# Kernel tuning notes

Hardware: AMD Instinct MI355X
Metric: run time of the kernel (lower is better)

The kernel has to match this reference:

```python
import jax, jax.numpy as jnp
import numpy as np

B, DIM_IN, DIM_OUT, K, EMBED, N, S = 32, 32, 32, 2, 16, 2048, 12


def setup_inputs() -> dict:
    key = jax.random.key(0)
    ks = jax.random.split(key, 12)
    sc = 0.1
    return {
        "x": jax.random.normal(ks[0], (B, DIM_IN, N, S), dtype=jnp.float32),
        "node_embeddings": jax.random.normal(ks[1], (N, EMBED), dtype=jnp.float32),
        "node_embeddings2": jax.random.normal(ks[2], (N, EMBED), dtype=jnp.float32),
        "weights_pool": jax.random.normal(ks[3], (EMBED, K + 1, DIM_IN, DIM_OUT), dtype=jnp.float32) * sc,
        "weights_pool2": jax.random.normal(ks[4], (EMBED, K + 1, DIM_IN, DIM_OUT), dtype=jnp.float32) * sc,
        "bias_pool": jax.random.normal(ks[5], (EMBED, DIM_OUT), dtype=jnp.float32) * sc,
        "bias_pool2": jax.random.normal(ks[6], (EMBED, DIM_OUT), dtype=jnp.float32) * sc,
        "fc0_w": jax.random.normal(ks[7], (1, S), dtype=jnp.float32) * sc,
        "fc0_b": jnp.zeros((1,), dtype=jnp.float32),
        "fc1_w": jax.random.normal(ks[8], (EMBED, N), dtype=jnp.float32) * sc,
        "fc1_b": jnp.zeros((EMBED,), dtype=jnp.float32),
        "fc2_w": jax.random.normal(ks[9], (EMBED, DIM_IN), dtype=jnp.float32) * sc,
        "fc2_b": jnp.zeros((EMBED,), dtype=jnp.float32),
    }


def _mlp(x, fc0_w, fc0_b, fc1_w, fc1_b, fc2_w, fc2_b):
    # x: [B, i, n, s] -> use first batch element, as in the torch code
    h = x[0]                                        # [i, n, s]
    h = jnp.tanh((h @ fc0_w.T + fc0_b).squeeze(-1))  # [i, n]
    h = jnp.tanh(h @ fc1_w.T + fc1_b)                # [i, d]
    h = h.T                                          # [d, i]
    h = jnp.tanh(h @ fc2_w.T + fc2_b)                # [d, d]
    return h


def reference(x, node_embeddings, node_embeddings2, weights_pool, weights_pool2,
              bias_pool, bias_pool2, fc0_w, fc0_b, fc1_w, fc1_b, fc2_w, fc2_b):
    m = _mlp(x, fc0_w, fc0_b, fc1_w, fc1_b, fc2_w, fc2_b)          # [d, d]
    logits = jax.nn.relu((node_embeddings @ m) @ node_embeddings2.T)  # [n, n]
    support = jax.nn.softmax(logits, axis=1)                        # [n, n]

    # k-hop powers of the dynamic adjacency (k is a small static int)
    support_set = [jnp.eye(N, dtype=support.dtype)]
    for _ in range(K):
        support_set.append(support_set[-1] @ support)
    supports = jnp.stack(support_set, axis=0)                       # [K+1, n, n]

    # node-embedding-generated weights and bias
    weights = (jnp.einsum('nd,dkio->nkio', node_embeddings, weights_pool)
               + jnp.einsum('nd,dkio->nkio', node_embeddings2, weights_pool2))  # [n,K+1,i,o]
    bias = node_embeddings @ bias_pool + node_embeddings2 @ bias_pool2          # [n, o]

    x_g = jnp.einsum('knm,bims->bknis', supports, x)                # [b,K+1,n,i,s]
    x_gconv = jnp.einsum('bknis,nkio->bsno', x_g, weights) + bias   # [b,s,n,o]
    out = jnp.transpose(x_gconv, (0, 3, 2, 1))                      # [b,o,n,s]
    # dropout is identity in eval mode
    return out
```

## Files before the change

### kernel.cpp

```cpp
#include <hip/hip_runtime.h>


typedef float  f32x4  __attribute__((ext_vector_type(4)));
typedef __bf16 bf16x8 __attribute__((ext_vector_type(8)));
typedef unsigned short u16;

#define GLOAD16(gp, lp) __builtin_amdgcn_global_load_lds( \
    (const __attribute__((address_space(1))) void*)(gp),  \
    (__attribute__((address_space(3))) void*)(lp), 16, 0, 0)

__device__ __forceinline__ u16 f2bf(float f){
  union { float f; unsigned u; } v; v.f = f;
  unsigned u = v.u;
  u += 0x7fffu + ((u >> 16) & 1u);
  return (u16)(u >> 16);
}
__device__ __forceinline__ float bf2f(u16 h){
  union { unsigned u; float f; } v; v.u = ((unsigned)h) << 16;
  return v.f;
}
__device__ __forceinline__ float2 unp2(unsigned u){
  union { unsigned q; float f; } a, b;
  a.q = u << 16; b.q = u & 0xffff0000u;
  return make_float2(a.f, b.f);
}

__global__ void k_h1(const float* __restrict__ x, const float* __restrict__ fc0w,
                     const float* __restrict__ fc0b, float* __restrict__ h1){
  int g = blockIdx.x * 256 + threadIdx.x;
  const float* xp = x + (long)g * 12;
  float s = fc0b[0];
  #pragma unroll
  for (int j = 0; j < 12; j++) s += xp[j] * fc0w[j];
  h1[g] = tanhf(s);
}

__global__ __launch_bounds__(256) void k_h2a(const float* __restrict__ h1,
                                             const float* __restrict__ fc1w,
                                             float* __restrict__ h2raw){
  __shared__ float red[4];
  int id = blockIdx.x;
  int i = id >> 4, d = id & 15;
  int t = threadIdx.x;
  const float* hp = h1 + i * 2048;
  const float* wp = fc1w + d * 2048;
  float s = 0.f;
  for (int nn = t; nn < 2048; nn += 256) s += hp[nn] * wp[nn];
  for (int off = 32; off > 0; off >>= 1) s += __shfl_down(s, off, 64);
  if ((t & 63) == 0) red[t >> 6] = s;
  __syncthreads();
  if (t == 0) h2raw[id] = red[0] + red[1] + red[2] + red[3];
}

__global__ void k_h2b(const float* __restrict__ h2raw, const float* __restrict__ fc1b,
                      const float* __restrict__ fc2w, const float* __restrict__ fc2b,
                      float* __restrict__ mmat){
  __shared__ float h2[512];
  int t = threadIdx.x;
  {
    int d = t & 15;
    h2[t] = tanhf(h2raw[t] + fc1b[d]);
  }
  __syncthreads();
  if (t < 256){
    int dd = t >> 4, e = t & 15;
    float s2 = fc2b[e];
    #pragma unroll
    for (int ii = 0; ii < 32; ii++) s2 += h2[ii * 16 + dd] * fc2w[e * 32 + ii];
    mmat[dd * 16 + e] = tanhf(s2);
  }
}

__global__ __launch_bounds__(256) void k_support(const float* __restrict__ E1,
                                                 const float* __restrict__ E2,
                                                 const float* __restrict__ mmat,
                                                 u16* __restrict__ sup){
  __shared__ float ml[256];
  __shared__ float tv[16];
  __shared__ float red[8];
  int n = blockIdx.x, t = threadIdx.x;
  ml[t] = mmat[t];
  __syncthreads();
  if (t < 16){
    float s = 0.f;
    const float* er = E1 + n * 16;
    #pragma unroll
    for (int d = 0; d < 16; d++) s += er[d] * ml[d * 16 + t];
    tv[t] = s;
  }
  __syncthreads();
  float lmax = -1e30f;
  float lv[8];
  #pragma unroll
  for (int p = 0; p < 8; p++){
    int j = t + p * 256;
    const float* e2 = E2 + j * 16;
    float s = 0.f;
    #pragma unroll
    for (int d = 0; d < 16; d++) s += tv[d] * e2[d];
    s = fmaxf(s, 0.f);
    lv[p] = s;
    lmax = fmaxf(lmax, s);
  }
  for (int off = 32; off > 0; off >>= 1) lmax = fmaxf(lmax, __shfl_down(lmax, off, 64));
  if ((t & 63) == 0) red[t >> 6] = lmax;
  __syncthreads();
  if (t == 0) red[0] = fmaxf(fmaxf(red[0], red[1]), fmaxf(red[2], red[3]));
  __syncthreads();
  float mx = red[0];
  float lsum = 0.f;
  #pragma unroll
  for (int p = 0; p < 8; p++){ float e = __expf(lv[p] - mx); lv[p] = e; lsum += e; }
  for (int off = 32; off > 0; off >>= 1) lsum += __shfl_down(lsum, off, 64);
  if ((t & 63) == 0) red[4 + (t >> 6)] = lsum;
  __syncthreads();
  if (t == 0) red[4] = red[4] + red[5] + red[6] + red[7];
  __syncthreads();
  float inv = 1.f / red[4];
  #pragma unroll
  for (int p = 0; p < 8; p++) sup[(long)n * 2048 + t + p * 256] = f2bf(lv[p] * inv);
}

__global__ void k_xb(const float* __restrict__ x, u16* __restrict__ Xb){
  int idx = blockIdx.x * 256 + threadIdx.x;
  int m = idx / 12288;
  int c = idx - m * 12288;
  int bi = c / 12, s = c - bi * 12;
  Xb[idx] = f2bf(x[((long)bi * 2048 + m) * 12 + s]);
}

__global__ __launch_bounds__(256) void k_xbt(const u16* __restrict__ Xb,
                                             u16* __restrict__ Xbt){
  __shared__ u16 tile[64][65];
  int cT = blockIdx.x * 64;
  int mT = blockIdx.y * 64;
  int t = threadIdx.x;
  int r = t >> 6, cc = t & 63;
  #pragma unroll
  for (int p = 0; p < 16; p++){
    int rr = p * 4 + r;
    tile[rr][cc] = Xb[(long)(mT + rr) * 12288 + cT + cc];
  }
  __syncthreads();
  #pragma unroll
  for (int p = 0; p < 16; p++){
    int rr = p * 4 + r;
    Xbt[(long)(cT + rr) * 2048 + mT + cc] = tile[cc][rr];
  }
}

__global__ void k_wb(const float* __restrict__ E1, const float* __restrict__ E2,
                     const float* __restrict__ P1, const float* __restrict__ P2,
                     const float* __restrict__ BP1, const float* __restrict__ BP2,
                     float* __restrict__ W, float* __restrict__ biasN){
  long g = (long)blockIdx.x * 256 + threadIdx.x;
  const long NW = (long)2048 * 3072;
  if (g < NW){
    int n = (int)(g / 3072), r = (int)(g - (long)n * 3072);
    const float* e1 = E1 + n * 16; const float* e2 = E2 + n * 16;
    float s = 0.f;
    #pragma unroll
    for (int d = 0; d < 16; d++) s += e1[d] * P1[d * 3072 + r] + e2[d] * P2[d * 3072 + r];
    W[g] = s;
  } else {
    long e = g - NW;
    if (e < 2048 * 32){
      int n = (int)(e >> 5), o = (int)(e & 31);
      const float* e1 = E1 + n * 16; const float* e2 = E2 + n * 16;
      float s = 0.f;
      #pragma unroll
      for (int d = 0; d < 16; d++) s += e1[d] * BP1[d * 32 + o] + e2[d] * BP2[d * 32 + o];
      biasN[e] = s;
    }
  }
}

__global__ __launch_bounds__(256) void k_gemm(const u16* __restrict__ A,
                                              const u16* __restrict__ Bt,
                                              u16* __restrict__ Cd,
                                              u16* __restrict__ Ct,
                                              int writeT){
  __shared__ u16 As[128 * 32];
  __shared__ u16 Bs[128 * 32];
  int tid  = threadIdx.x;
  int wave = tid >> 6, lane = tid & 63;
  int l15 = lane & 15, q = lane >> 4;
  int wm = wave >> 1, wc = wave & 1;
  long mBase = (long)blockIdx.y * 128;
  long cBase = (long)blockIdx.x * 128;
  f32x4 acc[4][4];
  #pragma unroll
  for (int t = 0; t < 4; t++)
    #pragma unroll
    for (int u = 0; u < 4; u++) acc[t][u] = (f32x4){0.f, 0.f, 0.f, 0.f};

  const u16* gA = A  + (mBase + wave * 16 + (lane >> 2)) * 2048 + (lane & 3) * 8;
  const u16* gB = Bt + (cBase + wave * 16 + (lane >> 2)) * 2048 + (lane & 3) * 8;
  u16* lA0 = As + wave * 512;
  u16* lA1 = As + 2048 + wave * 512;
  u16* lB0 = Bs + wave * 512;
  u16* lB1 = Bs + 2048 + wave * 512;

  for (int k0 = 0; k0 < 2048; k0 += 32){
    __syncthreads();
    GLOAD16(gA + k0,              lA0);
    GLOAD16(gA + 64 * 2048 + k0,  lA1);
    GLOAD16(gB + k0,              lB0);
    GLOAD16(gB + 64 * 2048 + k0,  lB1);
    __syncthreads();
    bf16x8 a[4], b[4];
    #pragma unroll
    for (int t = 0; t < 4; t++)
      a[t] = *(const bf16x8*)&As[(wm * 64 + t * 16 + l15) * 32 + q * 8];
    #pragma unroll
    for (int u = 0; u < 4; u++)
      b[u] = *(const bf16x8*)&Bs[(wc * 64 + u * 16 + l15) * 32 + q * 8];
    #pragma unroll
    for (int t = 0; t < 4; t++)
      #pragma unroll
      for (int u = 0; u < 4; u++)
        acc[t][u] = __builtin_amdgcn_mfma_f32_16x16x32_bf16(a[t], b[u], acc[t][u], 0, 0, 0);
  }
  #pragma unroll
  for (int t = 0; t < 4; t++){
    int mloc = wm * 64 + t * 16 + q * 4;
    #pragma unroll
    for (int u = 0; u < 4; u++){
      int cloc = wc * 64 + u * 16 + l15;
      long cg = cBase + cloc;
      long mg = mBase + mloc;
      u16 h0 = f2bf(acc[t][u][0]);
      u16 h1v = f2bf(acc[t][u][1]);
      u16 h2v = f2bf(acc[t][u][2]);
      u16 h3v = f2bf(acc[t][u][3]);
      Cd[(mg + 0) * 12288 + cg] = h0;
      Cd[(mg + 1) * 12288 + cg] = h1v;
      Cd[(mg + 2) * 12288 + cg] = h2v;
      Cd[(mg + 3) * 12288 + cg] = h3v;
      if (writeT){
        ushort4 v = make_ushort4(h0, h1v, h2v, h3v);
        *(ushort4*)&Ct[cg * 2048 + mg] = v;
      }
    }
  }
}

__global__ __launch_bounds__(256, 4) void k_final(const u16* __restrict__ G0,
                                                  const u16* __restrict__ G1,
                                                  const u16* __restrict__ G2,
                                                  const float* __restrict__ W,
                                                  const float* __restrict__ biasN,
                                                  float* __restrict__ out){
  __shared__ __align__(16) u16 gs[32 * 400];
  __shared__ __align__(16) float ws4[1024];
  __shared__ float bbuf[32];
  int bid = blockIdx.x;
  int n = (bid & 7) * 256 + (bid >> 3);
  int t = threadIdx.x;
  int b = t >> 3, oc = t & 7;
  f32x4 acc[4][3];
  #pragma unroll
  for (int jo = 0; jo < 4; jo++)
    #pragma unroll
    for (int v = 0; v < 3; v++) acc[jo][v] = (f32x4){0.f, 0.f, 0.f, 0.f};

  const u16* srcs[3] = {G0, G1, G2};
  for (int k = 0; k < 3; k++){
    __syncthreads();
    const uint4* src = (const uint4*)(srcs[k] + (long)n * 12288);
    #pragma unroll
    for (int p = 0; p < 6; p++){
      int c = t + p * 256;
      int br = c / 48, wi = c - br * 48;
      *(uint4*)&gs[br * 400 + wi * 8] = src[c];
    }
    const float4* wsrc = (const float4*)(W + (long)n * 3072 + k * 1024);
    *(float4*)&ws4[t * 4] = wsrc[t];
    if (k == 0 && t < 8) *(float4*)&bbuf[t * 4] = ((const float4*)(biasN + (long)n * 32))[t];
    __syncthreads();

    const u16* gp = gs + b * 400;
    #pragma unroll 4
    for (int ii = 0; ii < 16; ii++){
      uint4 A  = *(const uint4*)&gp[ii * 24];
      uint4 Bc = *(const uint4*)&gp[ii * 24 + 8];
      uint4 Cc = *(const uint4*)&gp[ii * 24 + 16];
      float2 p0 = unp2(A.x),  p1 = unp2(A.y),  p2 = unp2(A.z),  p3 = unp2(A.w);
      float2 p4 = unp2(Bc.x), p5 = unp2(Bc.y), p6 = unp2(Bc.z), p7 = unp2(Bc.w);
      float2 p8 = unp2(Cc.x), p9 = unp2(Cc.y), pa = unp2(Cc.z), pb = unp2(Cc.w);
      f32x4 G0v0 = (f32x4){p0.x, p0.y, p1.x, p1.y};
      f32x4 G0v1 = (f32x4){p2.x, p2.y, p3.x, p3.y};
      f32x4 G0v2 = (f32x4){p4.x, p4.y, p5.x, p5.y};
      f32x4 G1v0 = (f32x4){p6.x, p6.y, p7.x, p7.y};
      f32x4 G1v1 = (f32x4){p8.x, p8.y, p9.x, p9.y};
      f32x4 G1v2 = (f32x4){pa.x, pa.y, pb.x, pb.y};
      #pragma unroll
      for (int jo = 0; jo < 4; jo++){
        float w0 = ws4[(ii * 2)     * 32 + oc + jo * 8];
        float w1 = ws4[(ii * 2 + 1) * 32 + oc + jo * 8];
        acc[jo][0] += G0v0 * w0;
        acc[jo][1] += G0v1 * w0;
        acc[jo][2] += G0v2 * w0;
        acc[jo][0] += G1v0 * w1;
        acc[jo][1] += G1v1 * w1;
        acc[jo][2] += G1v2 * w1;
      }
    }
  }
  #pragma unroll
  for (int jo = 0; jo < 4; jo++){
    int o = oc + jo * 8;
    float bv = bbuf[o];
    f32x4 bs = {bv, bv, bv, bv};
    long base = ((long)(b * 32 + o) * 2048 + n) * 12;
    *(f32x4*)(out + base)     = acc[jo][0] + bs;
    *(f32x4*)(out + base + 4) = acc[jo][1] + bs;
    *(f32x4*)(out + base + 8) = acc[jo][2] + bs;
  }
}

extern "C" void kernel_launch(void* const* d_in, const int* in_sizes, int n_in,
                              void* d_out, int out_size, void* d_ws, size_t ws_size,
                              hipStream_t stream){
  const float* x    = (const float*)d_in[0];
  const float* E1   = (const float*)d_in[1];
  const float* E2   = (const float*)d_in[2];
  const float* P1   = (const float*)d_in[3];
  const float* P2   = (const float*)d_in[4];
  const float* BP1  = (const float*)d_in[5];
  const float* BP2  = (const float*)d_in[6];
  const float* fc0w = (const float*)d_in[7];
  const float* fc0b = (const float*)d_in[8];
  const float* fc1w = (const float*)d_in[9];
  const float* fc1b = (const float*)d_in[10];
  const float* fc2w = (const float*)d_in[11];
  const float* fc2b = (const float*)d_in[12];
  float* out = (float*)d_out;

  char* ws = (char*)d_ws;
  size_t off = 0;
  auto carve = [&](size_t bytes) -> char* {
    char* p = ws + off;
    off += (bytes + 255) & ~(size_t)255;
    return p;
  };
  float* h1            = (float*)carve((size_t)65536 * 4);
  float* h2raw         = (float*)carve((size_t)512 * 4);
  float* mmat          = (float*)carve((size_t)256 * 4);
  u16* sup             = (u16*)carve((size_t)2048 * 2048 * 2);
  u16* Xbt             = (u16*)carve((size_t)12288 * 2048 * 2);
  u16* Xb              = (u16*)carve((size_t)2048 * 12288 * 2);
  u16* G1t             = (u16*)carve((size_t)12288 * 2048 * 2);
  u16* G1              = (u16*)carve((size_t)2048 * 12288 * 2);
  float* W             = (float*)carve((size_t)2048 * 3072 * 4);
  float* biasN         = (float*)carve((size_t)2048 * 32 * 4);
  u16* G2              = Xbt;
  (void)ws_size; (void)in_sizes; (void)n_in; (void)out_size;

  k_h1     <<<256, 256, 0, stream>>>(x, fc0w, fc0b, h1);
  k_h2a    <<<512, 256, 0, stream>>>(h1, fc1w, h2raw);
  k_h2b    <<<1, 512, 0, stream>>>(h2raw, fc1b, fc2w, fc2b, mmat);
  k_support<<<2048, 256, 0, stream>>>(E1, E2, mmat, sup);
  k_xb     <<<98304, 256, 0, stream>>>(x, Xb);
  k_xbt    <<<dim3(192, 32), 256, 0, stream>>>(Xb, Xbt);
  k_wb     <<<24832, 256, 0, stream>>>(E1, E2, P1, P2, BP1, BP2, W, biasN);
  k_gemm   <<<dim3(96, 16), 256, 0, stream>>>(sup, Xbt, G1, G1t, 1);
  k_gemm   <<<dim3(96, 16), 256, 0, stream>>>(sup, G1t, G2, G1t, 0);
  k_final  <<<2048, 256, 0, stream>>>(Xb, G1, G2, W, biasN, out);
}
```

Baseline: 683.3 us.

## Deepen GEMM K-step, remap blocks across XCDs, stage epilogue through LDS

The bf16 MFMA GEMM now loads a K-slab of 64 per iteration instead of 32, which halves the number of barrier pairs. Block indices are remapped so that neighbouring column tiles are spread across the 8 XCDs while blocks sharing A rows stay grouped, aimed at better L2 reuse. The output tile is staged in a padded LDS buffer so that both the direct and transposed results go out as 16-byte coalesced stores instead of scattered 2-byte writes. The cost is a larger LDS footprint (about 34 KB), which may reduce occupancy, plus extra LDS traffic in the epilogue.

```diff
diff --git a/kernel.cpp b/kernel.cpp
--- a/kernel.cpp
+++ b/kernel.cpp
@@ -180,14 +180,20 @@
                                               u16* __restrict__ Cd,
                                               u16* __restrict__ Ct,
                                               int writeT){
-  __shared__ u16 As[128 * 32];
-  __shared__ u16 Bs[128 * 32];
+  __shared__ u16 lds[128 * 136];
   int tid  = threadIdx.x;
   int wave = tid >> 6, lane = tid & 63;
   int l15 = lane & 15, q = lane >> 4;
   int wm = wave >> 1, wc = wave & 1;
-  long mBase = (long)blockIdx.y * 128;
-  long cBase = (long)blockIdx.x * 128;
+
+  int lin  = blockIdx.y * 96 + blockIdx.x;
+  int xcd  = lin & 7;
+  int slot = lin >> 3;
+  int yN   = slot / 12;
+  int xN   = (slot - yN * 12) * 8 + xcd;
+  long mBase = (long)yN * 128;
+  long cBase = (long)xN * 128;
+
   f32x4 acc[4][4];
   #pragma unroll
   for (int t = 0; t < 4; t++)
@@ -196,52 +202,77 @@
 
   const u16* gA = A  + (mBase + wave * 16 + (lane >> 2)) * 2048 + (lane & 3) * 8;
   const u16* gB = Bt + (cBase + wave * 16 + (lane >> 2)) * 2048 + (lane & 3) * 8;
-  u16* lA0 = As + wave * 512;
-  u16* lA1 = As + 2048 + wave * 512;
-  u16* lB0 = Bs + wave * 512;
-  u16* lB1 = Bs + 2048 + wave * 512;
-
-  for (int k0 = 0; k0 < 2048; k0 += 32){
+  u16* lA = lds + wave * 512;
+  u16* lB = lds + 8192 + wave * 512;
+
+  for (int k0 = 0; k0 < 2048; k0 += 64){
     __syncthreads();
-    GLOAD16(gA + k0,              lA0);
-    GLOAD16(gA + 64 * 2048 + k0,  lA1);
-    GLOAD16(gB + k0,              lB0);
-    GLOAD16(gB + 64 * 2048 + k0,  lB1);
+    GLOAD16(gA + k0,                  lA);
+    GLOAD16(gA + 64 * 2048 + k0,      lA + 2048);
+    GLOAD16(gA + k0 + 32,             lA + 4096);
+    GLOAD16(gA + 64 * 2048 + k0 + 32, lA + 6144);
+    GLOAD16(gB + k0,                  lB);
+    GLOAD16(gB + 64 * 2048 + k0,      lB + 2048);
+    GLOAD16(gB + k0 + 32,             lB + 4096);
+    GLOAD16(gB + 64 * 2048 + k0 + 32, lB + 6144);
     __syncthreads();
     bf16x8 a[4], b[4];
     #pragma unroll
     for (int t = 0; t < 4; t++)
-      a[t] = *(const bf16x8*)&As[(wm * 64 + t * 16 + l15) * 32 + q * 8];
+      a[t] = *(const bf16x8*)&lds[(wm * 64 + t * 16 + l15) * 32 + q * 8];
     #pragma unroll
     for (int u = 0; u < 4; u++)
-      b[u] = *(const bf16x8*)&Bs[(wc * 64 + u * 16 + l15) * 32 + q * 8];
+      b[u] = *(const bf16x8*)&lds[8192 + (wc * 64 + u * 16 + l15) * 32 + q * 8];
     #pragma unroll
     for (int t = 0; t < 4; t++)
       #pragma unroll
       for (int u = 0; u < 4; u++)
         acc[t][u] = __builtin_amdgcn_mfma_f32_16x16x32_bf16(a[t], b[u], acc[t][u], 0, 0, 0);
-  }
+    #pragma unroll
+    for (int t = 0; t < 4; t++)
+      a[t] = *(const bf16x8*)&lds[4096 + (wm * 64 + t * 16 + l15) * 32 + q * 8];
+    #pragma unroll
+    for (int u = 0; u < 4; u++)
+      b[u] = *(const bf16x8*)&lds[12288 + (wc * 64 + u * 16 + l15) * 32 + q * 8];
+    #pragma unroll
+    for (int t = 0; t < 4; t++)
+      #pragma unroll
+      for (int u = 0; u < 4; u++)
+        acc[t][u] = __builtin_amdgcn_mfma_f32_16x16x32_bf16(a[t], b[u], acc[t][u], 0, 0, 0);
+  }
+
+  __syncthreads();
   #pragma unroll
   for (int t = 0; t < 4; t++){
     int mloc = wm * 64 + t * 16 + q * 4;
     #pragma unroll
     for (int u = 0; u < 4; u++){
       int cloc = wc * 64 + u * 16 + l15;
-      long cg = cBase + cloc;
-      long mg = mBase + mloc;
-      u16 h0 = f2bf(acc[t][u][0]);
-      u16 h1v = f2bf(acc[t][u][1]);
-      u16 h2v = f2bf(acc[t][u][2]);
-      u16 h3v = f2bf(acc[t][u][3]);
-      Cd[(mg + 0) * 12288 + cg] = h0;
-      Cd[(mg + 1) * 12288 + cg] = h1v;
-      Cd[(mg + 2) * 12288 + cg] = h2v;
-      Cd[(mg + 3) * 12288 + cg] = h3v;
-      if (writeT){
-        ushort4 v = make_ushort4(h0, h1v, h2v, h3v);
-        *(ushort4*)&Ct[cg * 2048 + mg] = v;
-      }
+      ushort4 v = make_ushort4(f2bf(acc[t][u][0]), f2bf(acc[t][u][1]),
+                               f2bf(acc[t][u][2]), f2bf(acc[t][u][3]));
+      *(ushort4*)&lds[cloc * 136 + mloc] = v;
     }
+  }
+  __syncthreads();
+  int rr = tid >> 4;
+  int ch = (tid & 15) * 8;
+  if (writeT){
+    #pragma unroll
+    for (int p = 0; p < 8; p++){
+      int r = p * 16 + rr;
+      uint4 v = *(const uint4*)&lds[r * 136 + ch];
+      *(uint4*)&Ct[(cBase + r) * 2048 + mBase + ch] = v;
+    }
+  }
+  #pragma unroll
+  for (int p = 0; p < 8; p++){
+    int m = p * 16 + rr;
+    unsigned w0 = (unsigned)lds[(ch + 0) * 136 + m] | ((unsigned)lds[(ch + 1) * 136 + m] << 16);
+    unsigned w1 = (unsigned)lds[(ch + 2) * 136 + m] | ((unsigned)lds[(ch + 3) * 136 + m] << 16);
+    unsigned w2 = (unsigned)lds[(ch + 4) * 136 + m] | ((unsigned)lds[(ch + 5) * 136 + m] << 16);
+    unsigned w3 = (unsigned)lds[(ch + 6) * 136 + m] | ((unsigned)lds[(ch + 7) * 136 + m] << 16);
+    uint4 v = make_uint4(w0, w1, w2, w3);
+    *(uint4*)&Cd[(mBase + m) * 12288 + cBase + ch] = v;
   }
 }
 
```

After: 663.6 us. 1.03x faster.
